# Performance work log

Measured on AMD Instinct MI355X. Metric: run time of the kernel, lower is better.

## Reference

```python
import jax, jax.numpy as jnp
import numpy as np

NKPT = 17      # keypooints (single dataset, dataset_idx=0)
M = 10         # num_in_class_proto
D = 768        # emb_dim (out_channels)
N = 131072     # samples
EPS = 0.05     # sinkhorn epsilon
ITERS = 3      # sinkhorn iterations
TAU = 0.5      # gumbel-softmax temperature
GAMMA = 0.999  # EMA momentum (update_weight=1.0 -> momentum=gamma)
CLAMP = 1e-4


def _l2n(x, axis=-1):
    # F.normalize(p=2) with eps guard
    return x / jnp.maximum(jnp.linalg.norm(x, axis=axis, keepdims=True), 1e-12)


def setup_inputs() -> dict:
    key = jax.random.key(0)
    k1, k2, k3, k4 = jax.random.split(key, 4)
    feats = jax.random.normal(k1, (N, D), dtype=jnp.float32)
    gt = jax.random.randint(k2, (N,), 0, NKPT)
    conf = jax.random.uniform(k3, (N,), dtype=jnp.float32)
    prototypes = _l2n(jax.random.normal(k4, (NKPT, M, D), dtype=jnp.float32) * 0.02)
    return {"feats": feats, "gt": gt, "conf": conf, "prototypes": prototypes}


def _sinkhorn_gumbel(logits, w, key):
    # logits: [N, M] rescaled similarities for one keypoint class
    # w: [N] 0/1 class-membership mask (emulates boolean-mask row selection:
    #    zeroed rows contribute nothing to the sinkhorn marginals)
    L = jnp.exp(logits / EPS) * w[:, None]                 # [N, M]
    B = jnp.sum(w)                                         # members
    L = L / jnp.sum(L)
    Kp = L.shape[1]
    for _ in range(ITERS):
        L = L / (jnp.sum(L, axis=0, keepdims=True) * Kp)   # per-prototype marginal
        col = jnp.sum(L, axis=1, keepdims=True)
        L = jnp.where(col > 0, L / (col * B), 0.0)         # per-sample marginal
    L = L * B
    idx = jnp.argmax(L, axis=1)                            # [N]
    # F.gumbel_softmax(L, tau=0.5, hard=True)
    g = jax.random.gumbel(key, L.shape, dtype=L.dtype)
    y_soft = jax.nn.softmax((L + g) / TAU, axis=-1)
    hard = jax.nn.one_hot(jnp.argmax(y_soft, axis=-1), Kp, dtype=y_soft.dtype)
    q = jax.lax.stop_gradient(hard - y_soft) + y_soft      # straight-through
    return q, idx


def _forward(feats, gt, conf, prototypes, key):
    feats = _l2n(feats)
    protos = _l2n(prototypes)                              # [K, M, D]
    sim = jnp.einsum('nd,kmd->nmk', feats, protos)         # [N, M, K]
    simr = jnp.abs(sim)                                    # sim_rescale='abs'
    out_cls = jnp.max(simr, axis=1)                        # [N, K]
    # --- prototype_learning ---
    sim2 = jnp.abs(feats @ protos.reshape(-1, D).T)        # [N, K*M]
    pred = jnp.argmax(out_cls, axis=1)
    conf_eff = jnp.where(gt == pred, conf, 0.0)            # conf[~mask] = 0
    proto_logits = sim2[:, : NKPT * M]
    members = (gt[None, :] == jnp.arange(NKPT)[:, None]).astype(feats.dtype)  # [K, N]
    init_q = jnp.transpose(simr, (2, 0, 1))                # [K, N, M]
    keys = jax.random.split(key, NKPT)
    qs, idxs = jax.vmap(_sinkhorn_gumbel)(init_q, members, keys)  # [K,N,M], [K,N]
    mk = conf_eff[None, :] * members                       # [K, N]
    # f = (q * m_k)^T @ (feats * m_k)  =>  conf enters squared, as in torch
    f = jnp.einsum('knm,kn,nd->kmd', qs, mk * mk, feats)   # [K, M, D]
    n = jnp.einsum('knm,kn->km', qs, mk)                   # [K, M]
    f = _l2n(f)
    valid = (n != 0)[..., None]                            # [K, M, 1]
    has = (jnp.sum(n, axis=1) > 0)[:, None, None]          # [K, 1, 1]
    new_protos = jnp.where(has & valid, GAMMA * protos + (1.0 - GAMMA) * f, protos)
    new_protos = _l2n(new_protos)
    # proto_target: cluster index within own gt class, offset by M*gt
    proto_target = jnp.take_along_axis(idxs, gt[None, :], axis=0)[0] + M * gt
    kpt_class = jnp.clip(out_cls, CLAMP, 1.0 - CLAMP)      # dataset_idx=0 slice is identity
    return proto_logits, proto_target, kpt_class, new_protos


def reference(feats, gt, conf, prototypes):
    return _forward(feats, gt, conf, prototypes, jax.random.key(42))
```

## Files before the change

### kernel.cpp

```cpp
#include <hip/hip_runtime.h>
#include <math.h>

#define NKPT 17
#define MM   10
#define DD   768
#define NN   131072
#define CC   (NKPT*MM)
#define CHUNKS 16
#define GCH2   4

typedef __bf16 bf16_t;
typedef bf16_t bf16x8 __attribute__((ext_vector_type(8)));
typedef float  f32x16 __attribute__((ext_vector_type(16)));

#define GLOAD_LDS16(g, s) \
    __builtin_amdgcn_global_load_lds((const __attribute__((address_space(1))) void*)(g), \
                                     (__attribute__((address_space(3))) void*)(s), 16, 0, 0)

__global__ __launch_bounds__(256) void k_proto_norm(const float* __restrict__ protos,
                                                    float* __restrict__ pn,
                                                    bf16_t* __restrict__ pnb) {
    int c = blockIdx.x;
    int t = threadIdx.x;
    if (c >= CC) {
        pnb[(size_t)c * DD + t]       = (bf16_t)0.f;
        pnb[(size_t)c * DD + t + 256] = (bf16_t)0.f;
        pnb[(size_t)c * DD + t + 512] = (bf16_t)0.f;
        return;
    }
    const float* row = protos + (size_t)c * DD;
    float v0 = row[t], v1 = row[t + 256], v2 = row[t + 512];
    double ss = (double)v0 * v0 + (double)v1 * v1 + (double)v2 * v2;
    __shared__ double red[256];
    red[t] = ss; __syncthreads();
    for (int s = 128; s > 0; s >>= 1) { if (t < s) red[t] += red[t + s]; __syncthreads(); }
    float invf = (float)(1.0 / fmax(sqrt(red[0]), 1e-12));
    float a0 = v0 * invf, a1 = v1 * invf, a2 = v2 * invf;
    pn[(size_t)c * DD + t]        = a0;
    pn[(size_t)c * DD + t + 256]  = a1;
    pn[(size_t)c * DD + t + 512]  = a2;
    pnb[(size_t)c * DD + t]       = (bf16_t)a0;
    pnb[(size_t)c * DD + t + 256] = (bf16_t)a1;
    pnb[(size_t)c * DD + t + 512] = (bf16_t)a2;
}

__global__ __launch_bounds__(256) void k_hist(const int* __restrict__ gt,
                                              int* __restrict__ counts) {
    __shared__ int c[NKPT];
    int t = threadIdx.x;
    if (t < NKPT) c[t] = 0;
    __syncthreads();
    for (int i = blockIdx.x * blockDim.x + t; i < NN; i += gridDim.x * blockDim.x)
        atomicAdd(&c[gt[i]], 1);
    __syncthreads();
    if (t < NKPT) atomicAdd(&counts[t], c[t]);
}

__global__ void k_prefix(const int* __restrict__ counts, int* __restrict__ offsets) {
    if (threadIdx.x == 0 && blockIdx.x == 0) {
        int acc = 0;
        for (int k = 0; k < NKPT; k++) { offsets[k] = acc; acc += counts[k]; }
        offsets[NKPT] = acc;
    }
}

__global__ __launch_bounds__(256) void k_rank(const int* __restrict__ gt,
                                              const int* __restrict__ offs,
                                              int* __restrict__ cursor,
                                              int* __restrict__ perm,
                                              int* __restrict__ rank) {
    __shared__ int cnt[NKPT], base[NKPT];
    int t = threadIdx.x;
    if (t < NKPT) cnt[t] = 0;
    __syncthreads();
    int n = blockIdx.x * 256 + t;
    int cls = gt[n];
    int lr = atomicAdd(&cnt[cls], 1);
    __syncthreads();
    if (t < NKPT) base[t] = atomicAdd(&cursor[t], cnt[t]);
    __syncthreads();
    int p = offs[cls] + base[cls] + lr;
    perm[p] = n;
    rank[n] = p;
}

__global__ __launch_bounds__(256) void k_prep(const float* __restrict__ feats,
                                              const float* __restrict__ pn,
                                              const int* __restrict__ gt,
                                              const int* __restrict__ perm,
                                              float* __restrict__ inv_f,
                                              double* __restrict__ Es,
                                              double* __restrict__ A) {
    __shared__ float pnS[MM * DD];
    int t = threadIdx.x, w = t >> 6, l = t & 63;
    int p0 = blockIdx.x * 32;
    int c0 = gt[perm[p0]];
    for (int idx = t; idx < MM * DD; idx += 256) pnS[idx] = pn[(size_t)c0 * (MM * DD) + idx];
    __syncthreads();
    double esum0 = 0.0, esum1 = 0.0;
    for (int g = 0; g < 2; g++) {
        int pg = p0 + w * 8 + g * 4;
        int nr[4], cl[4];
        bool uni = true;
        #pragma unroll
        for (int rr = 0; rr < 4; rr++) {
            nr[rr] = perm[pg + rr];
            cl[rr] = gt[nr[rr]];
            if (cl[rr] != c0) uni = false;
        }
        float4 fA[4][3];
        #pragma unroll
        for (int rr = 0; rr < 4; rr++) {
            const float4* r4 = (const float4*)(feats + (size_t)nr[rr] * DD);
            fA[rr][0] = r4[l]; fA[rr][1] = r4[l + 64]; fA[rr][2] = r4[l + 128];
        }
        double ss[4];
        #pragma unroll
        for (int rr = 0; rr < 4; rr++) {
            float4 a = fA[rr][0], b = fA[rr][1], c = fA[rr][2];
            ss[rr] = (double)a.x*a.x + (double)a.y*a.y + (double)a.z*a.z + (double)a.w*a.w
                   + (double)b.x*b.x + (double)b.y*b.y + (double)b.z*b.z + (double)b.w*b.w
                   + (double)c.x*c.x + (double)c.y*c.y + (double)c.z*c.z + (double)c.w*c.w;
        }
        #pragma unroll
        for (int st = 1; st < 64; st <<= 1)
            #pragma unroll
            for (int rr = 0; rr < 4; rr++) ss[rr] += __shfl_xor(ss[rr], st);
        float inv[4];
        #pragma unroll
        for (int rr = 0; rr < 4; rr++) inv[rr] = (float)(1.0 / fmax(sqrt(ss[rr]), 1e-12));
        if (l == 0) {
            #pragma unroll
            for (int rr = 0; rr < 4; rr++) inv_f[nr[rr]] = inv[rr];
        }
        float part[MM][4];
        if (uni) {
            #pragma unroll
            for (int m = 0; m < MM; m++) {
                const float4* P = (const float4*)(pnS + m * DD);
                float4 b0 = P[l], b1 = P[l + 64], b2 = P[l + 128];
                #pragma unroll
                for (int rr = 0; rr < 4; rr++) {
                    float4 a0 = fA[rr][0], a1 = fA[rr][1], a2 = fA[rr][2];
                    float v = a0.x*b0.x + a0.y*b0.y + a0.z*b0.z + a0.w*b0.w;
                    v = fmaf(a1.x, b1.x, v); v = fmaf(a1.y, b1.y, v);
                    v = fmaf(a1.z, b1.z, v); v = fmaf(a1.w, b1.w, v);
                    v = fmaf(a2.x, b2.x, v); v = fmaf(a2.y, b2.y, v);
                    v = fmaf(a2.z, b2.z, v); v = fmaf(a2.w, b2.w, v);
                    part[m][rr] = v;
                }
            }
        } else {
            #pragma unroll
            for (int m = 0; m < MM; m++) {
                #pragma unroll
                for (int rr = 0; rr < 4; rr++) {
                    const float4* P = (const float4*)(pn + (size_t)cl[rr] * (MM * DD) + m * DD);
                    float4 b0 = P[l], b1 = P[l + 64], b2 = P[l + 128];
                    float4 a0 = fA[rr][0], a1 = fA[rr][1], a2 = fA[rr][2];
                    float v = a0.x*b0.x + a0.y*b0.y + a0.z*b0.z + a0.w*b0.w;
                    v = fmaf(a1.x, b1.x, v); v = fmaf(a1.y, b1.y, v);
                    v = fmaf(a1.z, b1.z, v); v = fmaf(a1.w, b1.w, v);
                    v = fmaf(a2.x, b2.x, v); v = fmaf(a2.y, b2.y, v);
                    v = fmaf(a2.z, b2.z, v); v = fmaf(a2.w, b2.w, v);
                    part[m][rr] = v;
                }
            }
        }
        #pragma unroll
        for (int st = 1; st < 64; st <<= 1)
            #pragma unroll
            for (int m = 0; m < MM; m++)
                #pragma unroll
                for (int rr = 0; rr < 4; rr++) part[m][rr] += __shfl_xor(part[m][rr], st);
        if (l < MM) {
            #pragma unroll
            for (int rr = 0; rr < 4; rr++) {
                float v = part[0][rr];
                #pragma unroll
                for (int m = 1; m < MM; m++) v = (l == m) ? part[m][rr] : v;
                float sf = fabsf(v * inv[rr]);
                double es = exp(20.0 * (double)sf);
                Es[(size_t)(pg + rr) * MM + l] = es;
                if (cl[rr] == c0) esum0 += es; else esum1 += es;
            }
        }
    }
    __shared__ double colA[4][2][MM];
    if (l < MM) { colA[w][0][l] = esum0; colA[w][1][l] = esum1; }
    __syncthreads();
    if (t < 2 * MM) {
        int sel = t / MM, m = t - sel * MM;
        double v = colA[0][sel][m] + colA[1][sel][m] + colA[2][sel][m] + colA[3][sel][m];
        int cls = sel ? gt[perm[p0 + 31]] : c0;
        if ((sel == 0 || cls != c0) && v != 0.0) atomicAdd(&A[cls * MM + m], v);
    }
}

__global__ __launch_bounds__(256, 2) void k_gemm(const float* __restrict__ feats,
                                                 const bf16_t* __restrict__ pnb,
                                                 const float* __restrict__ inv_f,
                                                 float* __restrict__ o0) {
    __shared__ float  AsF[128 * 64];
    __shared__ bf16_t Bs[192 * 64];
    __shared__ float  sInv[128];
    int tid = threadIdx.x;
    int w = tid >> 6, l = tid & 63;
    int row0 = blockIdx.x * 128;
    if (tid < 128) sInv[tid] = inv_f[row0 + tid];
    f32x16 acc[6];
    #pragma unroll
    for (int ct = 0; ct < 6; ct++)
        #pragma unroll
        for (int i = 0; i < 16; i++) acc[ct][i] = 0.f;
    char* AsB = (char*)AsF;
    char* BsB = (char*)Bs;
    int am = l & 31, q = l >> 5;
    for (int kc = 0; kc < DD; kc += 64) {
        #pragma unroll
        for (int rep = 0; rep < 8; rep++) {
            int rg = w * 8 + rep;
            int r  = rg * 4 + (l >> 4);
            int cg = (l & 15) ^ (r & 15);
            const float* gp = feats + (size_t)(row0 + r) * DD + kc + cg * 4;
            GLOAD_LDS16(gp, AsB + rg * 1024);
        }
        #pragma unroll
        for (int rep = 0; rep < 6; rep++) {
            int rg = w * 6 + rep;
            int r  = rg * 8 + (l >> 3);
            int cg = (l & 7) ^ (r & 7);
            const bf16_t* gp = pnb + (size_t)r * DD + kc + cg * 8;
            GLOAD_LDS16(gp, BsB + rg * 1024);
        }
        __syncthreads();
        #pragma unroll
        for (int ks = 0; ks < 4; ks++) {
            int ar  = w * 32 + am;
            int c0a = ks * 4 + q * 2;
            int ca0 = (c0a)     ^ (ar & 15);
            int ca1 = (c0a + 1) ^ (ar & 15);
            float4 a0 = *(const float4*)(AsB + ar * 256 + ca0 * 16);
            float4 a1 = *(const float4*)(AsB + ar * 256 + ca1 * 16);
            bf16x8 af;
            af[0] = (bf16_t)a0.x; af[1] = (bf16_t)a0.y; af[2] = (bf16_t)a0.z; af[3] = (bf16_t)a0.w;
            af[4] = (bf16_t)a1.x; af[5] = (bf16_t)a1.y; af[6] = (bf16_t)a1.z; af[7] = (bf16_t)a1.w;
            #pragma unroll
            for (int ct = 0; ct < 6; ct++) {
                int br = ct * 32 + am;
                int cb = (ks * 2 + q) ^ (br & 7);
                bf16x8 bf = *(const bf16x8*)(BsB + br * 128 + cb * 16);
                acc[ct] = __builtin_amdgcn_mfma_f32_32x32x16_bf16(af, bf, acc[ct], 0, 0, 0);
            }
        }
        __syncthreads();
    }
    #pragma unroll
    for (int ct = 0; ct < 6; ct++) {
        int col = ct * 32 + am;
        if (col < CC) {
            #pragma unroll
            for (int reg = 0; reg < 16; reg++) {
                int rl = w * 32 + (reg & 3) + 8 * (reg >> 2) + 4 * q;
                o0[(size_t)(row0 + rl) * CC + col] = fabsf(acc[ct][reg] * sInv[rl]);
            }
        }
    }
}

__global__ __launch_bounds__(256) void k_epi2(const float* __restrict__ o0,
                                              const int* __restrict__ gt,
                                              const float* __restrict__ conf,
                                              const float* __restrict__ inv_f,
                                              const int* __restrict__ rank,
                                              float* __restrict__ o2,
                                              float* __restrict__ wq_s,
                                              float* __restrict__ wn_s) {
    __shared__ float S[64][CC + 1];
    int t = threadIdx.x;
    int row0 = blockIdx.x * 64;
    for (int idx = t; idx < 64 * CC; idx += 256) {
        int r = idx / CC, c = idx - r * CC;
        S[r][c] = o0[(size_t)(row0 + r) * CC + c];
    }
    __syncthreads();
    if (t < 64) {
        int n = row0 + t;
        float best = -1.f; int pred = 0;
        #pragma unroll
        for (int k = 0; k < NKPT; k++) {
            float mx = S[t][k * MM];
            #pragma unroll
            for (int m = 1; m < MM; m++) mx = fmaxf(mx, S[t][k * MM + m]);
            o2[(size_t)n * NKPT + k] = fminf(fmaxf(mx, 1e-4f), 1.f - 1e-4f);
            if (mx > best) { best = mx; pred = k; }
        }
        int cls = gt[n];
        float ce = (pred == cls) ? conf[n] : 0.f;
        int pos = rank[n];
        wq_s[pos] = ce * ce * inv_f[n];
        wn_s[pos] = ce;
    }
}

__global__ __launch_bounds__(256) void k_iter(const double* __restrict__ Es,
                                              const int* __restrict__ offsets,
                                              const int* __restrict__ counts,
                                              const double* __restrict__ Ain,
                                              int first,
                                              double* __restrict__ T) {
    int k  = blockIdx.x / CHUNKS;
    int ch = blockIdx.x % CHUNKS;
    int t = threadIdx.x;
    __shared__ double cfS[MM];
    __shared__ double sred[256];
    sred[t] = (t < CC) ? Ain[t] : 0.0;
    __syncthreads();
    if (first) {
        for (int s = 128; s > 0; s >>= 1) { if (t < s) sred[t] += sred[t + s]; __syncthreads(); }
        if (t < MM) cfS[t] = sred[0] / (10.0 * Ain[k * MM + t]);
    } else {
        if (t < MM) cfS[t] = 1.0 / (10.0 * Ain[k * MM + t]);
    }
    __syncthreads();
    int j0 = offsets[k], j1 = offsets[k + 1];
    long long len = j1 - j0;
    int c0 = j0 + (int)(len * ch / CHUNKS);
    int c1 = j0 + (int)(len * (ch + 1) / CHUNKS);
    double cf[MM];
    #pragma unroll
    for (int m = 0; m < MM; m++) cf[m] = cfS[m];
    double Bk = (double)counts[k];
    double acc[MM];
    #pragma unroll
    for (int m = 0; m < MM; m++) acc[m] = 0.0;
    for (int j = c0 + t; j < c1; j += 256) {
        double e[MM], rs = 0.0;
        #pragma unroll
        for (int m = 0; m < MM; m++) { e[m] = Es[(size_t)j * MM + m]; rs += e[m] * cf[m]; }
        double rowf = 1.0 / (Bk * rs);
        #pragma unroll
        for (int m = 0; m < MM; m++) acc[m] += e[m] * rowf;
    }
    __shared__ double red[4][MM];
    int lane = t & 63, w = t >> 6;
    #pragma unroll
    for (int m = 0; m < MM; m++) {
        double v = acc[m];
        for (int off = 32; off > 0; off >>= 1) v += __shfl_down(v, off);
        if (lane == 0) red[w][m] = v;
    }
    __syncthreads();
    if (t < MM) atomicAdd(&T[k * MM + t], red[0][t] + red[1][t] + red[2][t] + red[3][t]);
}

__global__ __launch_bounds__(256) void k_argmax(const double* __restrict__ Es,
                                                const int* __restrict__ offsets,
                                                const double* __restrict__ T2,
                                                const int* __restrict__ perm,
                                                const float* __restrict__ wq_s,
                                                float* __restrict__ o1,
                                                int* __restrict__ assign,
                                                int* __restrict__ ccnt) {
    int k  = blockIdx.x / CHUNKS;
    int ch = blockIdx.x % CHUNKS;
    int t = threadIdx.x;
    __shared__ double cfS[MM];
    if (t < MM) cfS[t] = 1.0 / (10.0 * T2[k * MM + t]);
    __syncthreads();
    int j0 = offsets[k], j1 = offsets[k + 1];
    long long len = j1 - j0;
    int c0 = j0 + (int)(len * ch / CHUNKS);
    int c1 = j0 + (int)(len * (ch + 1) / CHUNKS);
    double cf[MM];
    #pragma unroll
    for (int m = 0; m < MM; m++) cf[m] = cfS[m];
    for (int j = c0 + t; j < c1; j += 256) {
        double bestv = Es[(size_t)j * MM] * cf[0];
        int bi = 0;
        #pragma unroll
        for (int m = 1; m < MM; m++) {
            double v = Es[(size_t)j * MM + m] * cf[m];
            if (v > bestv) { bestv = v; bi = m; }
        }
        o1[perm[j]] = (float)(bi + MM * k);
        assign[j] = bi;
        if (wq_s[j] != 0.f) atomicAdd(&ccnt[k * MM + bi], 1);
    }
}

__global__ __launch_bounds__(256) void k_scatter(const int* __restrict__ offsets,
                                                 const int* __restrict__ perm,
                                                 const int* __restrict__ assign,
                                                 const float* __restrict__ wq_s,
                                                 const float* __restrict__ wn_s,
                                                 const int* __restrict__ ccnt,
                                                 int* __restrict__ ccur,
                                                 int* __restrict__ midx,
                                                 float* __restrict__ mw,
                                                 float* __restrict__ mn) {
    int k  = blockIdx.x / CHUNKS;
    int ch = blockIdx.x % CHUNKS;
    int t = threadIdx.x;
    __shared__ int cls_[CC];
    __shared__ int cbase[CC];
    if (t < CC) cls_[t] = ccnt[t];
    __syncthreads();
    if (t == 0) {
        int acc = 0;
        for (int i = 0; i < CC; i++) { cbase[i] = acc; acc += cls_[i]; }
    }
    __syncthreads();
    int j0 = offsets[k], j1 = offsets[k + 1];
    long long len = j1 - j0;
    int c0 = j0 + (int)(len * ch / CHUNKS);
    int c1 = j0 + (int)(len * (ch + 1) / CHUNKS);
    for (int j = c0 + t; j < c1; j += 256) {
        float wv = wq_s[j];
        if (wv != 0.f) {
            int c = k * MM + assign[j];
            int pos = atomicAdd(&ccur[c], 1);
            int dst = cbase[c] + pos;
            midx[dst] = perm[j];
            mw[dst]   = wv;
            mn[dst]   = wn_s[j];
        }
    }
}

__global__ __launch_bounds__(256) void k_gather2(const float* __restrict__ feats,
                                                 const int* __restrict__ ccnt,
                                                 const int* __restrict__ midx,
                                                 const float* __restrict__ mw,
                                                 const float* __restrict__ mn,
                                                 float* __restrict__ f_raw,
                                                 float* __restrict__ nkm) {
    int c = blockIdx.x;
    int ch = blockIdx.y;
    int t = threadIdx.x;
    __shared__ int cls_[CC];
    __shared__ int sb[2];
    if (t < CC) cls_[t] = ccnt[t];
    __syncthreads();
    if (t == 0) {
        int acc = 0;
        for (int i = 0; i < c; i++) acc += cls_[i];
        sb[0] = acc; sb[1] = cls_[c];
    }
    __syncthreads();
    int base = sb[0], cnt = sb[1];
    int s = base + (int)((long long)cnt * ch / GCH2);
    int e = base + (int)((long long)cnt * (ch + 1) / GCH2);
    __shared__ int   rls[256];
    __shared__ float wls[256];
    float a00=0.f,a01=0.f,a02=0.f,a03=0.f;
    float a10=0.f,a11=0.f,a12=0.f,a13=0.f;
    float a20=0.f,a21=0.f,a22=0.f,a23=0.f;
    float nacc = 0.f;
    for (int jb = s; jb < e; jb += 256) {
        int j = jb + t;
        if (j < e) { rls[t] = midx[j]; wls[t] = mw[j]; nacc += mn[j]; }
        __syncthreads();
        int lim = min(256, e - jb);
        int i = 0;
        for (; i + 4 <= lim; i += 4) {
            int r0 = rls[i], r1 = rls[i+1], r2 = rls[i+2], r3 = rls[i+3];
            float w0 = wls[i], w1 = wls[i+1], w2 = wls[i+2], w3 = wls[i+3];
            const float* p0 = feats + (size_t)r0 * DD;
            const float* p1 = feats + (size_t)r1 * DD;
            const float* p2 = feats + (size_t)r2 * DD;
            const float* p3 = feats + (size_t)r3 * DD;
            a00 = fmaf(w0, p0[t],       a00); a01 = fmaf(w1, p1[t],       a01);
            a02 = fmaf(w2, p2[t],       a02); a03 = fmaf(w3, p3[t],       a03);
            a10 = fmaf(w0, p0[t + 256], a10); a11 = fmaf(w1, p1[t + 256], a11);
            a12 = fmaf(w2, p2[t + 256], a12); a13 = fmaf(w3, p3[t + 256], a13);
            a20 = fmaf(w0, p0[t + 512], a20); a21 = fmaf(w1, p1[t + 512], a21);
            a22 = fmaf(w2, p2[t + 512], a22); a23 = fmaf(w3, p3[t + 512], a23);
        }
        for (; i < lim; i++) {
            int r0 = rls[i]; float w0 = wls[i];
            const float* p0 = feats + (size_t)r0 * DD;
            a00 = fmaf(w0, p0[t],       a00);
            a10 = fmaf(w0, p0[t + 256], a10);
            a20 = fmaf(w0, p0[t + 512], a20);
        }
        __syncthreads();
    }
    float a0 = (a00 + a01) + (a02 + a03);
    float a1 = (a10 + a11) + (a12 + a13);
    float a2 = (a20 + a21) + (a22 + a23);
    if (e > s) {
        atomicAdd(&f_raw[(size_t)c * DD + t],       a0);
        atomicAdd(&f_raw[(size_t)c * DD + t + 256], a1);
        atomicAdd(&f_raw[(size_t)c * DD + t + 512], a2);
    }
    __shared__ float nred[256];
    nred[t] = nacc; __syncthreads();
    for (int st = 128; st > 0; st >>= 1) { if (t < st) nred[t] += nred[t + st]; __syncthreads(); }
    if (t == 0 && nred[0] != 0.f) atomicAdd(&nkm[c], nred[0]);
}

__global__ __launch_bounds__(256) void k_newproto(const float* __restrict__ f_raw,
                                                  const float* __restrict__ nkm,
                                                  const float* __restrict__ pn,
                                                  float* __restrict__ o3) {
    int c = blockIdx.x, t = threadIdx.x;
    int k = c / MM;
    float f0 = f_raw[(size_t)c * DD + t];
    float f1 = f_raw[(size_t)c * DD + t + 256];
    float f2 = f_raw[(size_t)c * DD + t + 512];
    __shared__ double red[256];
    red[t] = (double)f0 * f0 + (double)f1 * f1 + (double)f2 * f2;
    __syncthreads();
    for (int s = 128; s > 0; s >>= 1) { if (t < s) red[t] += red[t + s]; __syncthreads(); }
    float invf = (float)(1.0 / fmax(sqrt(red[0]), 1e-12));
    bool valid = (nkm[c] != 0.f);
    float hs = 0.f;
    #pragma unroll
    for (int m = 0; m < MM; m++) hs += nkm[k * MM + m];
    bool has = (hs > 0.f);
    float p0 = pn[(size_t)c * DD + t];
    float p1 = pn[(size_t)c * DD + t + 256];
    float p2 = pn[(size_t)c * DD + t + 512];
    float v0, v1, v2;
    if (has && valid) {
        v0 = 0.999f * p0 + 0.001f * (f0 * invf);
        v1 = 0.999f * p1 + 0.001f * (f1 * invf);
        v2 = 0.999f * p2 + 0.001f * (f2 * invf);
    } else { v0 = p0; v1 = p1; v2 = p2; }
    __syncthreads();
    red[t] = (double)v0 * v0 + (double)v1 * v1 + (double)v2 * v2;
    __syncthreads();
    for (int s = 128; s > 0; s >>= 1) { if (t < s) red[t] += red[t + s]; __syncthreads(); }
    float inv2 = (float)(1.0 / fmax(sqrt(red[0]), 1e-12));
    o3[(size_t)c * DD + t]       = v0 * inv2;
    o3[(size_t)c * DD + t + 256] = v1 * inv2;
    o3[(size_t)c * DD + t + 512] = v2 * inv2;
}

extern "C" void kernel_launch(void* const* d_in, const int* in_sizes, int n_in,
                              void* d_out, int out_size, void* d_ws, size_t ws_size,
                              hipStream_t stream) {
    const float* feats  = (const float*)d_in[0];
    const int*   gt     = (const int*)d_in[1];
    const float* conf   = (const float*)d_in[2];
    const float* protos = (const float*)d_in[3];

    float* o0 = (float*)d_out;
    float* o1 = o0 + (size_t)NN * CC;
    float* o2 = o1 + NN;
    float* o3 = o2 + (size_t)NN * NKPT;

    char* ws = (char*)d_ws;
    float*  inv_f  = (float*)(ws + 0);
    float*  pn     = (float*)(ws + 524288);
    bf16_t* pnb    = (bf16_t*)(ws + 1048576);
    float*  wq_s   = (float*)(ws + 1441792);
    float*  wn_s   = (float*)(ws + 1966080);
    int*    perm   = (int*)  (ws + 2490368);
    int*    rka    = (int*)  (ws + 3014656);
    double* Es     = (double*)(ws + 3538944);
    char*   zz     = ws + 14024704;
    int*    counts = (int*)   (zz + 0);
    int*    cursor = (int*)   (zz + 128);
    int*    offs   = (int*)   (zz + 256);
    double* A      = (double*)(zz + 384);
    double* T1     = (double*)(zz + 2432);
    double* T2     = (double*)(zz + 4480);
    int*    ccnt   = (int*)   (zz + 6528);
    int*    ccur   = (int*)   (zz + 7296);
    float*  nkm    = (float*) (zz + 8064);
    float*  f_raw  = (float*) (zz + 8832);
    size_t  zz_bytes = 8832 + (size_t)CC * DD * 4;
    int*    midx   = (int*)  (ws + 16777216);
    float*  mw     = (float*)(ws + 17301504);
    float*  mn     = (float*)(ws + 17825792);

    hipMemsetAsync(zz, 0, zz_bytes, stream);
    k_proto_norm<<<192, 256, 0, stream>>>(protos, pn, pnb);
    k_hist<<<512, 256, 0, stream>>>(gt, counts);
    k_prefix<<<1, 64, 0, stream>>>(counts, offs);
    k_rank<<<NN / 256, 256, 0, stream>>>(gt, offs, cursor, perm, rka);
    k_prep<<<NN / 32, 256, 0, stream>>>(feats, pn, gt, perm, inv_f, Es, A);
    k_gemm<<<NN / 128, 256, 0, stream>>>(feats, pnb, inv_f, o0);
    k_epi2<<<NN / 64, 256, 0, stream>>>(o0, gt, conf, inv_f, rka, o2, wq_s, wn_s);
    k_iter<<<NKPT * CHUNKS, 256, 0, stream>>>(Es, offs, counts, A, 1, T1);
    k_iter<<<NKPT * CHUNKS, 256, 0, stream>>>(Es, offs, counts, T1, 0, T2);
    k_argmax<<<NKPT * CHUNKS, 256, 0, stream>>>(Es, offs, T2, perm, wq_s, o1, rka, ccnt);
    k_scatter<<<NKPT * CHUNKS, 256, 0, stream>>>(offs, perm, rka, wq_s, wn_s, ccnt, ccur, midx, mw, mn);
    dim3 gg(CC, GCH2);
    k_gather2<<<gg, 256, 0, stream>>>(feats, ccnt, midx, mw, mn, f_raw, nkm);
    k_newproto<<<CC, 256, 0, stream>>>(f_raw, nkm, pn, o3);
}
```

Before: 874.9 us.

## Fuse prep into split-bf16 MFMA GEMM and compute exp scores in its epilogue

Removes the separate k_prep kernel, which re-read all feats and did an fp32 dot product against the own-class prototypes. k_gemm now also computes the row norms and writes the exp(20*sim) entries for each sample's own class straight from its epilogue. To keep near-fp32 accuracy for those Sinkhorn inputs, both operands are split into bf16 hi/lo parts and the GEMM issues four MFMAs per tile, with the row tile halved to 64. A new k_colsumA kernel rebuilds the per-class column sums. The cost is four times the MFMA work plus extra LDS traffic in the GEMM, in exchange for dropping one full pass over feats.

```diff
diff --git a/kernel.cpp b/kernel.cpp
--- a/kernel.cpp
+++ b/kernel.cpp
@@ -19,13 +19,16 @@
 
 __global__ __launch_bounds__(256) void k_proto_norm(const float* __restrict__ protos,
                                                     float* __restrict__ pn,
-                                                    bf16_t* __restrict__ pnb) {
+                                                    bf16_t* __restrict__ pnbh,
+                                                    bf16_t* __restrict__ pnbl) {
     int c = blockIdx.x;
     int t = threadIdx.x;
     if (c >= CC) {
-        pnb[(size_t)c * DD + t]       = (bf16_t)0.f;
-        pnb[(size_t)c * DD + t + 256] = (bf16_t)0.f;
-        pnb[(size_t)c * DD + t + 512] = (bf16_t)0.f;
+        #pragma unroll
+        for (int s = 0; s < 3; s++) {
+            pnbh[(size_t)c * DD + t + s * 256] = (bf16_t)0.f;
+            pnbl[(size_t)c * DD + t + s * 256] = (bf16_t)0.f;
+        }
         return;
     }
     const float* row = protos + (size_t)c * DD;
@@ -39,9 +42,14 @@
     pn[(size_t)c * DD + t]        = a0;
     pn[(size_t)c * DD + t + 256]  = a1;
     pn[(size_t)c * DD + t + 512]  = a2;
-    pnb[(size_t)c * DD + t]       = (bf16_t)a0;
-    pnb[(size_t)c * DD + t + 256] = (bf16_t)a1;
-    pnb[(size_t)c * DD + t + 512] = (bf16_t)a2;
+    float av[3] = {a0, a1, a2};
+    #pragma unroll
+    for (int s = 0; s < 3; s++) {
+        bf16_t h = (bf16_t)av[s];
+        bf16_t lo = (bf16_t)(av[s] - (float)h);
+        pnbh[(size_t)c * DD + t + s * 256] = h;
+        pnbl[(size_t)c * DD + t + s * 256] = lo;
+    }
 }
 
 __global__ __launch_bounds__(256) void k_hist(const int* __restrict__ gt,
@@ -84,185 +92,106 @@
     rank[n] = p;
 }
 
-__global__ __launch_bounds__(256) void k_prep(const float* __restrict__ feats,
-                                              const float* __restrict__ pn,
-                                              const int* __restrict__ gt,
-                                              const int* __restrict__ perm,
-                                              float* __restrict__ inv_f,
-                                              double* __restrict__ Es,
-                                              double* __restrict__ A) {
-    __shared__ float pnS[MM * DD];
-    int t = threadIdx.x, w = t >> 6, l = t & 63;
-    int p0 = blockIdx.x * 32;
-    int c0 = gt[perm[p0]];
-    for (int idx = t; idx < MM * DD; idx += 256) pnS[idx] = pn[(size_t)c0 * (MM * DD) + idx];
-    __syncthreads();
-    double esum0 = 0.0, esum1 = 0.0;
-    for (int g = 0; g < 2; g++) {
-        int pg = p0 + w * 8 + g * 4;
-        int nr[4], cl[4];
-        bool uni = true;
-        #pragma unroll
-        for (int rr = 0; rr < 4; rr++) {
-            nr[rr] = perm[pg + rr];
-            cl[rr] = gt[nr[rr]];
-            if (cl[rr] != c0) uni = false;
-        }
-        float4 fA[4][3];
-        #pragma unroll
-        for (int rr = 0; rr < 4; rr++) {
-            const float4* r4 = (const float4*)(feats + (size_t)nr[rr] * DD);
-            fA[rr][0] = r4[l]; fA[rr][1] = r4[l + 64]; fA[rr][2] = r4[l + 128];
-        }
-        double ss[4];
-        #pragma unroll
-        for (int rr = 0; rr < 4; rr++) {
-            float4 a = fA[rr][0], b = fA[rr][1], c = fA[rr][2];
-            ss[rr] = (double)a.x*a.x + (double)a.y*a.y + (double)a.z*a.z + (double)a.w*a.w
-                   + (double)b.x*b.x + (double)b.y*b.y + (double)b.z*b.z + (double)b.w*b.w
-                   + (double)c.x*c.x + (double)c.y*c.y + (double)c.z*c.z + (double)c.w*c.w;
-        }
-        #pragma unroll
-        for (int st = 1; st < 64; st <<= 1)
-            #pragma unroll
-            for (int rr = 0; rr < 4; rr++) ss[rr] += __shfl_xor(ss[rr], st);
-        float inv[4];
-        #pragma unroll
-        for (int rr = 0; rr < 4; rr++) inv[rr] = (float)(1.0 / fmax(sqrt(ss[rr]), 1e-12));
-        if (l == 0) {
-            #pragma unroll
-            for (int rr = 0; rr < 4; rr++) inv_f[nr[rr]] = inv[rr];
-        }
-        float part[MM][4];
-        if (uni) {
-            #pragma unroll
-            for (int m = 0; m < MM; m++) {
-                const float4* P = (const float4*)(pnS + m * DD);
-                float4 b0 = P[l], b1 = P[l + 64], b2 = P[l + 128];
-                #pragma unroll
-                for (int rr = 0; rr < 4; rr++) {
-                    float4 a0 = fA[rr][0], a1 = fA[rr][1], a2 = fA[rr][2];
-                    float v = a0.x*b0.x + a0.y*b0.y + a0.z*b0.z + a0.w*b0.w;
-                    v = fmaf(a1.x, b1.x, v); v = fmaf(a1.y, b1.y, v);
-                    v = fmaf(a1.z, b1.z, v); v = fmaf(a1.w, b1.w, v);
-                    v = fmaf(a2.x, b2.x, v); v = fmaf(a2.y, b2.y, v);
-                    v = fmaf(a2.z, b2.z, v); v = fmaf(a2.w, b2.w, v);
-                    part[m][rr] = v;
-                }
-            }
-        } else {
-            #pragma unroll
-            for (int m = 0; m < MM; m++) {
-                #pragma unroll
-                for (int rr = 0; rr < 4; rr++) {
-                    const float4* P = (const float4*)(pn + (size_t)cl[rr] * (MM * DD) + m * DD);
-                    float4 b0 = P[l], b1 = P[l + 64], b2 = P[l + 128];
-                    float4 a0 = fA[rr][0], a1 = fA[rr][1], a2 = fA[rr][2];
-                    float v = a0.x*b0.x + a0.y*b0.y + a0.z*b0.z + a0.w*b0.w;
-                    v = fmaf(a1.x, b1.x, v); v = fmaf(a1.y, b1.y, v);
-                    v = fmaf(a1.z, b1.z, v); v = fmaf(a1.w, b1.w, v);
-                    v = fmaf(a2.x, b2.x, v); v = fmaf(a2.y, b2.y, v);
-                    v = fmaf(a2.z, b2.z, v); v = fmaf(a2.w, b2.w, v);
-                    part[m][rr] = v;
-                }
-            }
-        }
-        #pragma unroll
-        for (int st = 1; st < 64; st <<= 1)
-            #pragma unroll
-            for (int m = 0; m < MM; m++)
-                #pragma unroll
-                for (int rr = 0; rr < 4; rr++) part[m][rr] += __shfl_xor(part[m][rr], st);
-        if (l < MM) {
-            #pragma unroll
-            for (int rr = 0; rr < 4; rr++) {
-                float v = part[0][rr];
-                #pragma unroll
-                for (int m = 1; m < MM; m++) v = (l == m) ? part[m][rr] : v;
-                float sf = fabsf(v * inv[rr]);
-                double es = exp(20.0 * (double)sf);
-                Es[(size_t)(pg + rr) * MM + l] = es;
-                if (cl[rr] == c0) esum0 += es; else esum1 += es;
-            }
-        }
-    }
-    __shared__ double colA[4][2][MM];
-    if (l < MM) { colA[w][0][l] = esum0; colA[w][1][l] = esum1; }
-    __syncthreads();
-    if (t < 2 * MM) {
-        int sel = t / MM, m = t - sel * MM;
-        double v = colA[0][sel][m] + colA[1][sel][m] + colA[2][sel][m] + colA[3][sel][m];
-        int cls = sel ? gt[perm[p0 + 31]] : c0;
-        if ((sel == 0 || cls != c0) && v != 0.0) atomicAdd(&A[cls * MM + m], v);
-    }
-}
-
 __global__ __launch_bounds__(256, 2) void k_gemm(const float* __restrict__ feats,
-                                                 const bf16_t* __restrict__ pnb,
-                                                 const float* __restrict__ inv_f,
+                                                 const bf16_t* __restrict__ pnbh,
+                                                 const bf16_t* __restrict__ pnbl,
+                                                 const int* __restrict__ gt,
+                                                 const int* __restrict__ rank,
+                                                 float* __restrict__ inv_f,
+                                                 double* __restrict__ Es,
                                                  float* __restrict__ o0) {
-    __shared__ float  AsF[128 * 64];
-    __shared__ bf16_t Bs[192 * 64];
-    __shared__ float  sInv[128];
+    __shared__ __align__(16) char pool[65536];
+    char* AsB = pool;
+    char* BhB = pool + 16384;
+    char* BlB = pool + 40960;
+    float* sInvL = (float*)(pool + 40960);
+    int*   sGt   = (int*)(pool + 41216);
+    int*   sRank = (int*)(pool + 41472);
     int tid = threadIdx.x;
     int w = tid >> 6, l = tid & 63;
-    int row0 = blockIdx.x * 128;
-    if (tid < 128) sInv[tid] = inv_f[row0 + tid];
-    f32x16 acc[6];
-    #pragma unroll
-    for (int ct = 0; ct < 6; ct++)
+    int row0 = blockIdx.x * 64;
+    int am = l & 31, q = l >> 5;
+    int mh2 = w & 1;
+    int ng  = w >> 1;
+    f32x16 acc[3];
+    #pragma unroll
+    for (int ct = 0; ct < 3; ct++)
         #pragma unroll
         for (int i = 0; i < 16; i++) acc[ct][i] = 0.f;
-    char* AsB = (char*)AsF;
-    char* BsB = (char*)Bs;
-    int am = l & 31, q = l >> 5;
+    double ss = 0.0;
+    int ar = mh2 * 32 + am;
     for (int kc = 0; kc < DD; kc += 64) {
         #pragma unroll
-        for (int rep = 0; rep < 8; rep++) {
-            int rg = w * 8 + rep;
+        for (int rep = 0; rep < 4; rep++) {
+            int rg = w * 4 + rep;
             int r  = rg * 4 + (l >> 4);
             int cg = (l & 15) ^ (r & 15);
-            const float* gp = feats + (size_t)(row0 + r) * DD + kc + cg * 4;
-            GLOAD_LDS16(gp, AsB + rg * 1024);
+            GLOAD_LDS16(feats + (size_t)(row0 + r) * DD + kc + cg * 4, AsB + rg * 1024);
         }
         #pragma unroll
         for (int rep = 0; rep < 6; rep++) {
             int rg = w * 6 + rep;
             int r  = rg * 8 + (l >> 3);
             int cg = (l & 7) ^ (r & 7);
-            const bf16_t* gp = pnb + (size_t)r * DD + kc + cg * 8;
-            GLOAD_LDS16(gp, BsB + rg * 1024);
+            GLOAD_LDS16(pnbh + (size_t)r * DD + kc + cg * 8, BhB + rg * 1024);
+            GLOAD_LDS16(pnbl + (size_t)r * DD + kc + cg * 8, BlB + rg * 1024);
         }
         __syncthreads();
         #pragma unroll
         for (int ks = 0; ks < 4; ks++) {
-            int ar  = w * 32 + am;
             int c0a = ks * 4 + q * 2;
-            int ca0 = (c0a)     ^ (ar & 15);
-            int ca1 = (c0a + 1) ^ (ar & 15);
-            float4 a0 = *(const float4*)(AsB + ar * 256 + ca0 * 16);
-            float4 a1 = *(const float4*)(AsB + ar * 256 + ca1 * 16);
-            bf16x8 af;
-            af[0] = (bf16_t)a0.x; af[1] = (bf16_t)a0.y; af[2] = (bf16_t)a0.z; af[3] = (bf16_t)a0.w;
-            af[4] = (bf16_t)a1.x; af[5] = (bf16_t)a1.y; af[6] = (bf16_t)a1.z; af[7] = (bf16_t)a1.w;
+            float4 a0 = *(const float4*)(AsB + ar * 256 + ((c0a)     ^ (ar & 15)) * 16);
+            float4 a1 = *(const float4*)(AsB + ar * 256 + ((c0a + 1) ^ (ar & 15)) * 16);
+            ss += (double)a0.x*a0.x + (double)a0.y*a0.y + (double)a0.z*a0.z + (double)a0.w*a0.w
+                + (double)a1.x*a1.x + (double)a1.y*a1.y + (double)a1.z*a1.z + (double)a1.w*a1.w;
+            bf16x8 ah, al;
+            { bf16_t h; float v;
+              v=a0.x; h=(bf16_t)v; ah[0]=h; al[0]=(bf16_t)(v-(float)h);
+              v=a0.y; h=(bf16_t)v; ah[1]=h; al[1]=(bf16_t)(v-(float)h);
+              v=a0.z; h=(bf16_t)v; ah[2]=h; al[2]=(bf16_t)(v-(float)h);
+              v=a0.w; h=(bf16_t)v; ah[3]=h; al[3]=(bf16_t)(v-(float)h);
+              v=a1.x; h=(bf16_t)v; ah[4]=h; al[4]=(bf16_t)(v-(float)h);
+              v=a1.y; h=(bf16_t)v; ah[5]=h; al[5]=(bf16_t)(v-(float)h);
+              v=a1.z; h=(bf16_t)v; ah[6]=h; al[6]=(bf16_t)(v-(float)h);
+              v=a1.w; h=(bf16_t)v; ah[7]=h; al[7]=(bf16_t)(v-(float)h); }
             #pragma unroll
-            for (int ct = 0; ct < 6; ct++) {
-                int br = ct * 32 + am;
-                int cb = (ks * 2 + q) ^ (br & 7);
-                bf16x8 bf = *(const bf16x8*)(BsB + br * 128 + cb * 16);
-                acc[ct] = __builtin_amdgcn_mfma_f32_32x32x16_bf16(af, bf, acc[ct], 0, 0, 0);
+            for (int ct = 0; ct < 3; ct++) {
+                int br = (ng * 3 + ct) * 32 + am;
+                int cb = ((ks * 2 + q) ^ (br & 7)) * 16;
+                bf16x8 bh = *(const bf16x8*)(BhB + br * 128 + cb);
+                bf16x8 bl = *(const bf16x8*)(BlB + br * 128 + cb);
+                acc[ct] = __builtin_amdgcn_mfma_f32_32x32x16_bf16(ah, bh, acc[ct], 0, 0, 0);
+                acc[ct] = __builtin_amdgcn_mfma_f32_32x32x16_bf16(ah, bl, acc[ct], 0, 0, 0);
+                acc[ct] = __builtin_amdgcn_mfma_f32_32x32x16_bf16(al, bh, acc[ct], 0, 0, 0);
+                acc[ct] = __builtin_amdgcn_mfma_f32_32x32x16_bf16(al, bl, acc[ct], 0, 0, 0);
             }
         }
         __syncthreads();
     }
-    #pragma unroll
-    for (int ct = 0; ct < 6; ct++) {
-        int col = ct * 32 + am;
+    ss += __shfl_xor(ss, 32);
+    float inv = (float)(1.0 / fmax(sqrt(ss), 1e-12));
+    if (w < 2 && q == 0) {
+        sInvL[mh2 * 32 + am] = inv;
+        inv_f[row0 + mh2 * 32 + am] = inv;
+    }
+    if (tid < 64) {
+        sGt[tid]   = gt[row0 + tid];
+        sRank[tid] = rank[row0 + tid];
+    }
+    __syncthreads();
+    #pragma unroll
+    for (int ct = 0; ct < 3; ct++) {
+        int col = (ng * 3 + ct) * 32 + am;
         if (col < CC) {
             #pragma unroll
             for (int reg = 0; reg < 16; reg++) {
-                int rl = w * 32 + (reg & 3) + 8 * (reg >> 2) + 4 * q;
-                o0[(size_t)(row0 + rl) * CC + col] = fabsf(acc[ct][reg] * sInv[rl]);
+                int rl = mh2 * 32 + (reg & 3) + 8 * (reg >> 2) + 4 * q;
+                float sv = fabsf(acc[ct][reg] * sInvL[rl]);
+                o0[(size_t)(row0 + rl) * CC + col] = sv;
+                int gtc = sGt[rl];
+                unsigned j = (unsigned)(col - gtc * MM);
+                if (j < (unsigned)MM)
+                    Es[(size_t)sRank[rl] * MM + j] = exp(20.0 * (double)sv);
             }
         }
     }
@@ -301,6 +230,35 @@
         wq_s[pos] = ce * ce * inv_f[n];
         wn_s[pos] = ce;
     }
+}
+
+__global__ __launch_bounds__(256) void k_colsumA(const double* __restrict__ Es,
+                                                 const int* __restrict__ offsets,
+                                                 double* __restrict__ A) {
+    int k  = blockIdx.x / CHUNKS;
+    int ch = blockIdx.x % CHUNKS;
+    int j0 = offsets[k], j1 = offsets[k + 1];
+    long long len = j1 - j0;
+    int c0 = j0 + (int)(len * ch / CHUNKS);
+    int c1 = j0 + (int)(len * (ch + 1) / CHUNKS);
+    int t = threadIdx.x;
+    double acc[MM];
+    #pragma unroll
+    for (int m = 0; m < MM; m++) acc[m] = 0.0;
+    for (int j = c0 + t; j < c1; j += 256) {
+        #pragma unroll
+        for (int m = 0; m < MM; m++) acc[m] += Es[(size_t)j * MM + m];
+    }
+    __shared__ double red[4][MM];
+    int lane = t & 63, w = t >> 6;
+    #pragma unroll
+    for (int m = 0; m < MM; m++) {
+        double v = acc[m];
+        for (int off = 32; off > 0; off >>= 1) v += __shfl_down(v, off);
+        if (lane == 0) red[w][m] = v;
+    }
+    __syncthreads();
+    if (t < MM) atomicAdd(&A[k * MM + t], red[0][t] + red[1][t] + red[2][t] + red[3][t]);
 }
 
 __global__ __launch_bounds__(256) void k_iter(const double* __restrict__ Es,
@@ -554,13 +512,14 @@
     char* ws = (char*)d_ws;
     float*  inv_f  = (float*)(ws + 0);
     float*  pn     = (float*)(ws + 524288);
-    bf16_t* pnb    = (bf16_t*)(ws + 1048576);
-    float*  wq_s   = (float*)(ws + 1441792);
-    float*  wn_s   = (float*)(ws + 1966080);
-    int*    perm   = (int*)  (ws + 2490368);
-    int*    rka    = (int*)  (ws + 3014656);
-    double* Es     = (double*)(ws + 3538944);
-    char*   zz     = ws + 14024704;
+    bf16_t* pnbh   = (bf16_t*)(ws + 1048576);
+    bf16_t* pnbl   = (bf16_t*)(ws + 1441792);
+    float*  wq_s   = (float*)(ws + 1835008);
+    float*  wn_s   = (float*)(ws + 2359296);
+    int*    perm   = (int*)  (ws + 2883584);
+    int*    rka    = (int*)  (ws + 3407872);
+    double* Es     = (double*)(ws + 3932160);
+    char*   zz     = ws + 14417920;
     int*    counts = (int*)   (zz + 0);
     int*    cursor = (int*)   (zz + 128);
     int*    offs   = (int*)   (zz + 256);
@@ -572,18 +531,18 @@
     float*  nkm    = (float*) (zz + 8064);
     float*  f_raw  = (float*) (zz + 8832);
     size_t  zz_bytes = 8832 + (size_t)CC * DD * 4;
-    int*    midx   = (int*)  (ws + 16777216);
-    float*  mw     = (float*)(ws + 17301504);
-    float*  mn     = (float*)(ws + 17825792);
+    int*    midx   = (int*)  (ws + 15728640);
+    float*  mw     = (float*)(ws + 16252928);
+    float*  mn     = (float*)(ws + 16777216);
 
     hipMemsetAsync(zz, 0, zz_bytes, stream);
-    k_proto_norm<<<192, 256, 0, stream>>>(protos, pn, pnb);
+    k_proto_norm<<<192, 256, 0, stream>>>(protos, pn, pnbh, pnbl);
     k_hist<<<512, 256, 0, stream>>>(gt, counts);
     k_prefix<<<1, 64, 0, stream>>>(counts, offs);
     k_rank<<<NN / 256, 256, 0, stream>>>(gt, offs, cursor, perm, rka);
-    k_prep<<<NN / 32, 256, 0, stream>>>(feats, pn, gt, perm, inv_f, Es, A);
-    k_gemm<<<NN / 128, 256, 0, stream>>>(feats, pnb, inv_f, o0);
+    k_gemm<<<NN / 64, 256, 0, stream>>>(feats, pnbh, pnbl, gt, rka, inv_f, Es, o0);
     k_epi2<<<NN / 64, 256, 0, stream>>>(o0, gt, conf, inv_f, rka, o2, wq_s, wn_s);
+    k_colsumA<<<NKPT * CHUNKS, 256, 0, stream>>>(Es, offs, A);
     k_iter<<<NKPT * CHUNKS, 256, 0, stream>>>(Es, offs, counts, A, 1, T1);
     k_iter<<<NKPT * CHUNKS, 256, 0, stream>>>(Es, offs, counts, T1, 0, T2);
     k_argmax<<<NKPT * CHUNKS, 256, 0, stream>>>(Es, offs, T2, perm, wq_s, o1, rka, ccnt);
```

New measurement: 719.4 us. 1.22x faster.
